# Kernel optimization log

Hardware: AMD Instinct MI355X
Metric: run time of the kernel (lower is better)

## Reference

```python
import jax, jax.numpy as jnp
import numpy as np

# Config mirroring the TF module: cross-attention path (one_on_rna == 2),
# use_attn_augument=1, aug_multiply=0, two_d_softm=1, two_d_softm_mul_row_count=1,
# reduce_level=20 (protok used for padding masks).
B, L, D, H = 4, 1024, 512, 8
DEPTH = D // H          # 64, matches the repeat(64) in padding_to_zeros
NEG = -1.0e9


def setup_inputs() -> dict:
    key = jax.random.key(0)
    ks = jax.random.split(key, 16)
    s = np.float32(1.0 / np.sqrt(D))  # glorot-ish scale
    q = jax.random.normal(ks[0], (B, L, D), jnp.float32)
    kv = jax.random.normal(ks[1], (B, L, D), jnp.float32)
    # protein tokens; 0 == padding (compared against 0.0 in the TF code)
    protok = jax.random.randint(ks[2], (B, L), 0, 21).astype(jnp.float32)
    statpot_hb = jax.random.uniform(ks[3], (B, L, L), dtype=jnp.float32)
    statpot_pi = jax.random.uniform(ks[4], (B, L, L), dtype=jnp.float32)
    # cross padding mask: 1.0 where the protein (query) position is padding
    pad = (protok == 0.0).astype(jnp.float32)            # [B, L]
    cross_mask = jnp.broadcast_to(pad[:, :, None], (B, L, L)).astype(jnp.float32)
    wq = jax.random.normal(ks[5], (D, D), jnp.float32) * s
    wk = jax.random.normal(ks[6], (D, D), jnp.float32) * s
    wv = jax.random.normal(ks[7], (D, D), jnp.float32) * s
    wo = jax.random.normal(ks[8], (D, D), jnp.float32) * s
    bq = jnp.zeros((D,), jnp.float32)
    bk = jnp.zeros((D,), jnp.float32)
    bv = jnp.zeros((D,), jnp.float32)
    bo = jnp.zeros((D,), jnp.float32)
    aug_weight_att = jnp.ones((1,), jnp.float32)
    aug_weight_aug = jnp.ones((1,), jnp.float32)
    return dict(q=q, kv=kv, protok=protok, statpot_hb=statpot_hb,
                statpot_pi=statpot_pi, cross_mask=cross_mask,
                wq=wq, bq=bq, wk=wk, bk=bk, wv=wv, bv=bv, wo=wo, bo=bo,
                aug_weight_att=aug_weight_att, aug_weight_aug=aug_weight_aug)


def _split_heads(x):
    # [B, L, D] -> [B, H, L, depth]
    return x.reshape(B, L, H, DEPTH).transpose(0, 2, 1, 3)


def reference(q, kv, protok, statpot_hb, statpot_pi, cross_mask,
              wq, bq, wk, bk, wv, bv, wo, bo, aug_weight_att, aug_weight_aug):
    # padding_to_zeros: zero features at padded protein positions
    pad_keep = (protok != 0.0).astype(q.dtype)[:, :, None]   # [B, L, 1]
    qp = (q @ wq + bq) * pad_keep   # query side is the protein (len == max_pro_len)
    k = kv @ wk + bk
    v = kv @ wv + bv
    qh, kh, vh = _split_heads(qp), _split_heads(k), _split_heads(v)

    # unscaled QK^T (original does NOT divide by sqrt(depth))
    logits = jnp.einsum('bhqd,bhkd->bhqk', qh, kh)           # [B,H,L,L]

    # statistical-potential augmentation (aug_multiply == 0 -> additive)
    table = jnp.stack([statpot_hb, statpot_pi], axis=1)      # [B,2,L,L]
    table = jnp.repeat(table, H // 2, axis=1)                # [B,H,L,L]
    logits = logits / jnp.max(logits)
    logits = aug_weight_att * logits
    table = aug_weight_aug * table
    table = table / jnp.max(table)
    logits = logits + table

    # additive large-negative mask, broadcast over heads
    logits = logits + cross_mask[:, None, :, :] * NEG

    # 2D softmax jointly over (query, key) axes
    attn = jax.nn.softmax(logits.reshape(B, H, L * L), axis=-1).reshape(B, H, L, L)

    # rescale by number of non-padded protein rows (two_d_softm_mul_row_count)
    mul = jnp.count_nonzero(protok, axis=1).astype(attn.dtype)[:, None, None, None]
    attn = attn * mul
    attn = attn / jnp.max(attn)

    # output = attn^T @ v : contracts the QUERY axis (as in the original matmul)
    out = jnp.einsum('bhqk,bhqd->bhkd', attn, vh)            # [B,H,L,depth]
    out = out.transpose(0, 2, 1, 3).reshape(B, L, D)
    out = out @ wo + bo
    out = out * pad_keep                                     # final padding zeroing
    return out
```

## Files before the change

### kernel.cpp

```cpp
#include <hip/hip_runtime.h>
#include <math.h>

#define BB 4
#define LL 1024
#define DD 512
#define HH 8
#define DEP 64
#define NEGV (-1.0e9f)

typedef __attribute__((ext_vector_type(8))) short bf16x8;
typedef __attribute__((ext_vector_type(4))) float f32x4;
typedef unsigned short u16;
typedef unsigned int u32;

#define S_GMAX 0
#define S_TMAX 1
#define S_TMIN 2
#define S_MUL  4
#define S_SUM  8
#define S_M    40
#define S_C    72
#define P_TMAX 128
#define P_TMIN 384
#define P_GMAX 640
#define SCAL_F 1152
#define PER_T  (BB*HH*LL*DEP)

__device__ inline u16 f2b(float x) {
  u32 u = __float_as_uint(x);
  return (u16)((u + 0x7FFFu + ((u >> 16) & 1u)) >> 16);
}
__device__ inline float b2f(u16 h) { return __uint_as_float(((u32)h) << 16); }

__device__ inline void atomicMaxF(float* addr, float val) {
  unsigned int* ua = (unsigned int*)addr;
  unsigned int old = *ua;
  while (__uint_as_float(old) < val) {
    unsigned int assumed = old;
    old = atomicCAS(ua, assumed, __float_as_uint(val));
    if (old == assumed) break;
  }
}

__global__ void k0_init(float* ws) {
  int t = threadIdx.x;
  if (t < 4)  ws[S_MUL + t] = 0.0f;
  if (t < 32) { ws[S_SUM + t] = 0.0f; ws[S_M + t] = -INFINITY; ws[S_C + t] = 0.0f; }
}

__global__ void k_count(const float* __restrict__ protok, float* ws) {
  int b = blockIdx.x;
  int cnt = 0;
  for (int l = threadIdx.x; l < LL; l += blockDim.x)
    cnt += (protok[b*LL + l] != 0.0f) ? 1 : 0;
  __shared__ int sh[4];
  int lane = threadIdx.x & 63, w = threadIdx.x >> 6;
  #pragma unroll
  for (int o = 32; o > 0; o >>= 1) cnt += __shfl_down(cnt, o);
  if (lane == 0) sh[w] = cnt;
  __syncthreads();
  if (threadIdx.x == 0) ws[S_MUL + b] = (float)(sh[0] + sh[1] + sh[2] + sh[3]);
}

__global__ __launch_bounds__(256) void k_tminmax(const float* __restrict__ hb,
                                                 const float* __restrict__ pi,
                                                 float* __restrict__ ws) {
  const int g = blockIdx.x*256 + threadIdx.x;
  float mx = -INFINITY, mn = INFINITY;
  #pragma unroll
  for (int rep = 0; rep < 4; ++rep) {
    float4 a[4], c[4];
    #pragma unroll
    for (int j = 0; j < 4; ++j) {
      size_t idx = (size_t)rep*262144 + (size_t)j*65536 + g;
      a[j] = ((const float4*)hb)[idx];
      c[j] = ((const float4*)pi)[idx];
    }
    #pragma unroll
    for (int j = 0; j < 4; ++j) {
      mx = fmaxf(mx, fmaxf(fmaxf(a[j].x, a[j].y), fmaxf(a[j].z, a[j].w)));
      mx = fmaxf(mx, fmaxf(fmaxf(c[j].x, c[j].y), fmaxf(c[j].z, c[j].w)));
      mn = fminf(mn, fminf(fminf(a[j].x, a[j].y), fminf(a[j].z, a[j].w)));
      mn = fminf(mn, fminf(fminf(c[j].x, c[j].y), fminf(c[j].z, c[j].w)));
    }
  }
  __shared__ float shx[4], shn[4];
  int lane = threadIdx.x & 63, w = threadIdx.x >> 6;
  #pragma unroll
  for (int o = 32; o > 0; o >>= 1) {
    mx = fmaxf(mx, __shfl_down(mx, o));
    mn = fminf(mn, __shfl_down(mn, o));
  }
  if (lane == 0) { shx[w] = mx; shn[w] = mn; }
  __syncthreads();
  if (threadIdx.x == 0) {
    ws[P_TMAX + blockIdx.x] = fmaxf(fmaxf(shx[0], shx[1]), fmaxf(shx[2], shx[3]));
    ws[P_TMIN + blockIdx.x] = fminf(fminf(shn[0], shn[1]), fminf(shn[2], shn[3]));
  }
}

__global__ void k_red(float* __restrict__ ws) {
  const int t = threadIdx.x;
  float gm = fmaxf(ws[P_GMAX + t], ws[P_GMAX + t + 256]);
  float tm = ws[P_TMAX + t];
  float tn = ws[P_TMIN + t];
  __shared__ float sg[4], st[4], sn[4];
  int lane = t & 63, w = t >> 6;
  #pragma unroll
  for (int o = 32; o > 0; o >>= 1) {
    gm = fmaxf(gm, __shfl_down(gm, o));
    tm = fmaxf(tm, __shfl_down(tm, o));
    tn = fminf(tn, __shfl_down(tn, o));
  }
  if (lane == 0) { sg[w] = gm; st[w] = tm; sn[w] = tn; }
  __syncthreads();
  if (t == 0) {
    ws[S_GMAX] = fmaxf(fmaxf(sg[0], sg[1]), fmaxf(sg[2], sg[3]));
    ws[S_TMAX] = fmaxf(fmaxf(st[0], st[1]), fmaxf(st[2], st[3]));
    ws[S_TMIN] = fminf(fminf(sn[0], sn[1]), fminf(sn[2], sn[3]));
  }
}

__global__ __launch_bounds__(256) void k_xb(const float* __restrict__ q,
                                            const float* __restrict__ kv,
                                            u16* __restrict__ Xb) {
  int tg = blockIdx.x*256 + threadIdx.x;
  int which = tg >> 18;
  size_t off8 = (size_t)(tg & 262143) * 8;
  const float* s = which ? kv : q;
  float4 f0 = *(const float4*)&s[off8];
  float4 f1 = *(const float4*)&s[off8 + 4];
  u32 p0 = (u32)f2b(f0.x) | ((u32)f2b(f0.y) << 16);
  u32 p1 = (u32)f2b(f0.z) | ((u32)f2b(f0.w) << 16);
  u32 p2 = (u32)f2b(f1.x) | ((u32)f2b(f1.y) << 16);
  u32 p3 = (u32)f2b(f1.z) | ((u32)f2b(f1.w) << 16);
  *(int4*)&Xb[(size_t)which*PER_T + off8] = make_int4(p0, p1, p2, p3);
}

__global__ __launch_bounds__(256) void k_wt(
    const float* __restrict__ wq, const float* __restrict__ wk,
    const float* __restrict__ wv, const float* __restrict__ wo,
    u16* __restrict__ WTb) {
  const int g = blockIdx.z;
  const float* W = (g==0)?wq:(g==1)?wk:(g==2)?wv:wo;
  const int k0 = blockIdx.x*64, n0 = blockIdx.y*64;
  __shared__ u16 Ls[64][72];
  const int t = threadIdx.x;
  {
    const int r = t>>2, c16 = (t&3)*16;
    float v[16];
    #pragma unroll
    for (int j=0;j<4;++j) {
      float4 f = *(const float4*)&W[(size_t)(k0+r)*DD + n0 + c16 + 4*j];
      v[4*j]=f.x; v[4*j+1]=f.y; v[4*j+2]=f.z; v[4*j+3]=f.w;
    }
    u32 pk_[8];
    #pragma unroll
    for (int j=0;j<8;++j) pk_[j] = (u32)f2b(v[2*j]) | ((u32)f2b(v[2*j+1])<<16);
    *(int4*)&Ls[r][c16]   = make_int4(pk_[0],pk_[1],pk_[2],pk_[3]);
    *(int4*)&Ls[r][c16+8] = make_int4(pk_[4],pk_[5],pk_[6],pk_[7]);
  }
  __syncthreads();
  {
    const int n = t>>2, kk = (t&3)*16;
    u16 u[16];
    #pragma unroll
    for (int j=0;j<16;++j) u[j] = Ls[kk+j][n];
    u32 q_[8];
    #pragma unroll
    for (int j=0;j<8;++j) q_[j] = (u32)u[2*j] | ((u32)u[2*j+1]<<16);
    size_t dst = ((size_t)(g*DD + n0 + n))*DD + k0 + kk;
    *(int4*)&WTb[dst]   = make_int4(q_[0],q_[1],q_[2],q_[3]);
    *(int4*)&WTb[dst+8] = make_int4(q_[4],q_[5],q_[6],q_[7]);
  }
}

__global__ __launch_bounds__(256) void k1_proj(
    const float* __restrict__ protok,
    const float* __restrict__ bq, const float* __restrict__ bk,
    const float* __restrict__ bv,
    const u16* __restrict__ Xb, const u16* __restrict__ WTb,
    u16* __restrict__ QPb, u16* __restrict__ KHb, u16* __restrict__ VTb) {
  const int gid = blockIdx.z;
  const u16* X = Xb + (gid == 0 ? 0 : (size_t)PER_T);
  const float* bia = (gid == 0) ? bq : (gid == 1) ? bk : bv;
  const int m0 = blockIdx.x*64;
  const int h  = blockIdx.y;
  __shared__ u16 As[64][72];
  __shared__ u16 Bs[64][72];
  const int t = threadIdx.x;
  const int w = t>>6, lane = t&63, i = lane&15, g2 = lane>>4;
  const int sr = t>>2, sc = (t&3)*16;

  f32x4 acc[4];
  #pragma unroll
  for (int ct=0;ct<4;++ct) acc[ct] = (f32x4){0.f,0.f,0.f,0.f};

  for (int kk0 = 0; kk0 < DD; kk0 += 64) {
    __syncthreads();
    {
      size_t sx = (size_t)(m0+sr)*DD + kk0 + sc;
      *(int4*)&As[sr][sc]   = *(const int4*)&X[sx];
      *(int4*)&As[sr][sc+8] = *(const int4*)&X[sx+8];
    }
    {
      size_t src = ((size_t)(gid*DD + h*64 + sr))*DD + kk0 + sc;
      *(int4*)&Bs[sr][sc]   = *(const int4*)&WTb[src];
      *(int4*)&Bs[sr][sc+8] = *(const int4*)&WTb[src+8];
    }
    __syncthreads();
    bf16x8 a0 = *(const bf16x8*)&As[16*w + i][g2*8];
    bf16x8 a1 = *(const bf16x8*)&As[16*w + i][32 + g2*8];
    #pragma unroll
    for (int ct=0; ct<4; ++ct) {
      bf16x8 b0 = *(const bf16x8*)&Bs[ct*16 + i][g2*8];
      bf16x8 b1 = *(const bf16x8*)&Bs[ct*16 + i][32 + g2*8];
      acc[ct] = __builtin_amdgcn_mfma_f32_16x16x32_bf16(a0, b0, acc[ct], 0,0,0);
      acc[ct] = __builtin_amdgcn_mfma_f32_16x16x32_bf16(a1, b1, acc[ct], 0,0,0);
    }
  }
  __syncthreads();
  const int lrow = 16*w + g2*4;
  if (gid == 2) {
    #pragma unroll
    for (int ct=0;ct<4;++ct)
      #pragma unroll
      for (int r=0;r<4;++r)
        As[lrow + r][ct*16 + i] = f2b(acc[ct][r] + bia[h*64 + ct*16 + i]);
    __syncthreads();
    const int b = m0 >> 10, l0 = m0 & 1023;
    const int d = t>>2, lc = (t&3)*16;
    u16 u[16];
    #pragma unroll
    for (int j=0;j<16;++j) u[j] = As[lc+j][d];
    u32 q_[8];
    #pragma unroll
    for (int j=0;j<8;++j) q_[j] = (u32)u[2*j] | ((u32)u[2*j+1]<<16);
    size_t dst = ((size_t)(b*HH + h)*DEP + d)*LL + l0 + lc;
    *(int4*)&VTb[dst]   = make_int4(q_[0],q_[1],q_[2],q_[3]);
    *(int4*)&VTb[dst+8] = make_int4(q_[4],q_[5],q_[6],q_[7]);
  } else {
    u16* Y = (gid == 0) ? QPb : KHb;
    #pragma unroll
    for (int ct=0;ct<4;++ct)
      #pragma unroll
      for (int r=0;r<4;++r) {
        int m = m0 + lrow + r;
        float keep = (gid == 0) ? ((protok[m] != 0.0f) ? 1.0f : 0.0f) : 1.0f;
        int b = m >> 10, l = m & 1023;
        float val = (acc[ct][r] + bia[h*64 + ct*16 + i]) * keep;
        Y[((size_t)(b*HH + h)*LL + l)*DEP + ct*16 + i] = f2b(val);
      }
  }
}

__global__ __launch_bounds__(256) void k3_gmax(
    const u16* __restrict__ QPb, const u16* __restrict__ KHb,
    float* __restrict__ wsf) {
  const int q0 = blockIdx.x*64, bh = blockIdx.y;
  __shared__ u16 Qs[64][72];
  __shared__ u16 Ks[2][64][72];
  const int t = threadIdx.x;
  const int w = t>>6, lane = t&63, i = lane&15, g2 = lane>>4;
  const int sr = t>>2, sc = (t&3)*16;
  const u16* Qb = QPb + (size_t)bh*LL*DEP;
  const u16* Kb = KHb + (size_t)bh*LL*DEP;
  {
    size_t sq = (size_t)(q0 + sr)*DEP + sc;
    *(int4*)&Qs[sr][sc]   = *(const int4*)&Qb[sq];
    *(int4*)&Qs[sr][sc+8] = *(const int4*)&Qb[sq+8];
  }
  int4 rn0 = *(const int4*)&Kb[(size_t)sr*DEP + sc];
  int4 rn1 = *(const int4*)&Kb[(size_t)sr*DEP + sc + 8];
  __syncthreads();
  *(int4*)&Ks[0][sr][sc]   = rn0;
  *(int4*)&Ks[0][sr][sc+8] = rn1;
  rn0 = *(const int4*)&Kb[(size_t)(64 + sr)*DEP + sc];
  rn1 = *(const int4*)&Kb[(size_t)(64 + sr)*DEP + sc + 8];
  __syncthreads();
  bf16x8 a0 = *(const bf16x8*)&Qs[16*w + i][g2*8];
  bf16x8 a1 = *(const bf16x8*)&Qs[16*w + i][32 + g2*8];
  float mx = -INFINITY;
  for (int kt = 0; kt < 16; ++kt) {
    const int cur = kt & 1;
    #pragma unroll
    for (int ct=0;ct<4;++ct) {
      bf16x8 b0 = *(const bf16x8*)&Ks[cur][ct*16 + i][g2*8];
      bf16x8 b1 = *(const bf16x8*)&Ks[cur][ct*16 + i][32 + g2*8];
      f32x4 z = (f32x4){0.f,0.f,0.f,0.f};
      z = __builtin_amdgcn_mfma_f32_16x16x32_bf16(a0, b0, z, 0,0,0);
      z = __builtin_amdgcn_mfma_f32_16x16x32_bf16(a1, b1, z, 0,0,0);
      mx = fmaxf(mx, fmaxf(fmaxf(z[0],z[1]), fmaxf(z[2],z[3])));
    }
    if (kt < 15) {
      __syncthreads();
      *(int4*)&Ks[cur^1][sr][sc]   = rn0;
      *(int4*)&Ks[cur^1][sr][sc+8] = rn1;
      if (kt < 14) {
        rn0 = *(const int4*)&Kb[(size_t)((kt+2)*64 + sr)*DEP + sc];
        rn1 = *(const int4*)&Kb[(size_t)((kt+2)*64 + sr)*DEP + sc + 8];
      }
      __syncthreads();
    }
  }
  __shared__ float red[4];
  #pragma unroll
  for (int o = 32; o > 0; o >>= 1) mx = fmaxf(mx, __shfl_down(mx, o));
  if (lane == 0) red[w] = mx;
  __syncthreads();
  if (t == 0)
    wsf[P_GMAX + bh*16 + blockIdx.x] = fmaxf(fmaxf(red[0],red[1]), fmaxf(red[2],red[3]));
}

__global__ __launch_bounds__(256) void k4_fused(
    const float* __restrict__ protok,
    const float* __restrict__ hb, const float* __restrict__ pi,
    const float* __restrict__ w_att, const float* __restrict__ w_aug,
    const u16* __restrict__ QPb, const u16* __restrict__ KHb,
    const u16* __restrict__ VTb, u16* __restrict__ Ob,
    float* __restrict__ wsf) {
  const int k0 = blockIdx.x*64;
  const int bh = blockIdx.y, b = bh>>3, h = bh&7;
  const float* tab = ((h < 4) ? hb : pi) + (size_t)b*LL*LL;
  const float gmax  = wsf[S_GMAX];
  const float tmaxr = wsf[S_TMAX], tminr = wsf[S_TMIN];
  const float wa = w_att[0], wg = w_aug[0];
  const float inv_g = wa / gmax;
  const float tden  = (wg >= 0.0f) ? (wg * tmaxr) : (wg * tminr);
  const float inv_t = wg / tden;

  __shared__ u16 Ks[64][72];
  __shared__ u16 Qs[64][72];
  __shared__ u16 Vt[64][72];
  __shared__ u16 Pt[64][72];
  const int t = threadIdx.x;
  const int w = t>>6, lane = t&63, i = lane&15, g2 = lane>>4;
  const int sr = t>>2, sc = (t&3)*16;
  const int qlb = 16*w + g2*4;

  {
    size_t sk = ((size_t)bh*LL + k0 + sr)*DEP + sc;
    *(int4*)&Ks[sr][sc]   = *(const int4*)&KHb[sk];
    *(int4*)&Ks[sr][sc+8] = *(const int4*)&KHb[sk+8];
  }
  int4 rq0 = *(const int4*)&QPb[((size_t)bh*LL + sr)*DEP + sc];
  int4 rq1 = *(const int4*)&QPb[((size_t)bh*LL + sr)*DEP + sc + 8];
  int4 rv0 = *(const int4*)&VTb[((size_t)bh*DEP + sr)*LL + sc];
  int4 rv1 = *(const int4*)&VTb[((size_t)bh*DEP + sr)*LL + sc + 8];
  float tvr[4][4];
  #pragma unroll
  for (int r=0;r<4;++r)
    #pragma unroll
    for (int ct=0;ct<4;++ct)
      tvr[r][ct] = tab[(size_t)(qlb + r)*LL + k0 + ct*16 + i];
  __syncthreads();
  bf16x8 kb0[4], kb1[4];
  #pragma unroll
  for (int ct=0;ct<4;++ct) {
    kb0[ct] = *(const bf16x8*)&Ks[ct*16 + i][g2*8];
    kb1[ct] = *(const bf16x8*)&Ks[ct*16 + i][32 + g2*8];
  }
  f32x4 accO[4];
  #pragma unroll
  for (int dt=0;dt<4;++dt) accO[dt] = (f32x4){0.f,0.f,0.f,0.f};
  float lsum = 0.0f, lmax = -INFINITY;

  for (int q0 = 0; q0 < LL; q0 += 64) {
    const bool more = (q0 + 64) < LL;
    __syncthreads();
    *(int4*)&Qs[sr][sc]   = rq0;
    *(int4*)&Qs[sr][sc+8] = rq1;
    *(int4*)&Vt[sr][sc]   = rv0;
    *(int4*)&Vt[sr][sc+8] = rv1;
    __syncthreads();
    if (more) {
      rq0 = *(const int4*)&QPb[((size_t)bh*LL + q0 + 64 + sr)*DEP + sc];
      rq1 = *(const int4*)&QPb[((size_t)bh*LL + q0 + 64 + sr)*DEP + sc + 8];
      rv0 = *(const int4*)&VTb[((size_t)bh*DEP + sr)*LL + q0 + 64 + sc];
      rv1 = *(const int4*)&VTb[((size_t)bh*DEP + sr)*LL + q0 + 64 + sc + 8];
    }
    bf16x8 a0 = *(const bf16x8*)&Qs[16*w + i][g2*8];
    bf16x8 a1 = *(const bf16x8*)&Qs[16*w + i][32 + g2*8];
    f32x4 s4[4];
    #pragma unroll
    for (int ct=0; ct<4; ++ct) {
      f32x4 z = (f32x4){0.f,0.f,0.f,0.f};
      z = __builtin_amdgcn_mfma_f32_16x16x32_bf16(a0, kb0[ct], z, 0,0,0);
      z = __builtin_amdgcn_mfma_f32_16x16x32_bf16(a1, kb1[ct], z, 0,0,0);
      s4[ct] = z;
    }
    float tv2[4][4];
    if (more) {
      #pragma unroll
      for (int r=0;r<4;++r)
        #pragma unroll
        for (int ct=0;ct<4;++ct)
          tv2[r][ct] = tab[(size_t)(q0 + 64 + qlb + r)*LL + k0 + ct*16 + i];
    }
    #pragma unroll
    for (int r=0;r<4;++r) {
      int qrow = q0 + qlb + r;
      float madd = (protok[b*LL + qrow] == 0.0f) ? NEGV : 0.0f;
      #pragma unroll
      for (int ct=0;ct<4;++ct) {
        float sp = s4[ct][r]*inv_g + tvr[r][ct]*inv_t + madd;
        lmax = fmaxf(lmax, sp);
        float p = __expf(sp);
        lsum += p;
        Pt[ct*16 + i][qlb + r] = f2b(p);
      }
    }
    __syncthreads();
    bf16x8 pa0 = *(const bf16x8*)&Pt[16*w + i][g2*8];
    bf16x8 pa1 = *(const bf16x8*)&Pt[16*w + i][32 + g2*8];
    #pragma unroll
    for (int dt=0; dt<4; ++dt) {
      bf16x8 v0 = *(const bf16x8*)&Vt[dt*16 + i][g2*8];
      bf16x8 v1 = *(const bf16x8*)&Vt[dt*16 + i][32 + g2*8];
      accO[dt] = __builtin_amdgcn_mfma_f32_16x16x32_bf16(pa0, v0, accO[dt], 0,0,0);
      accO[dt] = __builtin_amdgcn_mfma_f32_16x16x32_bf16(pa1, v1, accO[dt], 0,0,0);
    }
    if (more) {
      #pragma unroll
      for (int r=0;r<4;++r)
        #pragma unroll
        for (int ct=0;ct<4;++ct) tvr[r][ct] = tv2[r][ct];
    }
  }
  #pragma unroll
  for (int dt=0;dt<4;++dt)
    #pragma unroll
    for (int r=0;r<4;++r)
      Ob[((size_t)bh*LL + k0 + qlb + r)*DEP + dt*16 + i] = f2b(accO[dt][r]);
  __shared__ float rs[4], rm[4];
  #pragma unroll
  for (int o = 32; o > 0; o >>= 1) {
    lsum += __shfl_down(lsum, o);
    lmax = fmaxf(lmax, __shfl_down(lmax, o));
  }
  if (lane == 0) { rs[w] = lsum; rm[w] = lmax; }
  __syncthreads();
  if (t == 0) {
    atomicAdd(&wsf[S_SUM + bh], rs[0]+rs[1]+rs[2]+rs[3]);
    atomicMaxF(&wsf[S_M + bh], fmaxf(fmaxf(rm[0], rm[1]), fmaxf(rm[2], rm[3])));
  }
}

__global__ void k45_cbh(float* ws) {
  int t = threadIdx.x;
  __shared__ float a_sh[32];
  if (t < 32) {
    int b = t >> 3;
    float s = ws[S_SUM + t], m = ws[S_M + t], mul = ws[S_MUL + b];
    a_sh[t] = mul * __expf(m) / s;
  }
  __syncthreads();
  if (t < 32) {
    float amax = -INFINITY;
    #pragma unroll
    for (int i = 0; i < 32; ++i) amax = fmaxf(amax, a_sh[i]);
    int b = t >> 3;
    float s = ws[S_SUM + t], mul = ws[S_MUL + b];
    ws[S_C + t] = (mul / s) / amax;
  }
}

__global__ __launch_bounds__(256) void k5_out(
    const float* __restrict__ protok,
    const float* __restrict__ bo,
    const u16* __restrict__ WTb, const u16* __restrict__ Ob,
    const float* __restrict__ wsf, float* __restrict__ out) {
  const int m0 = blockIdx.x*64, n0 = blockIdx.y*64;
  const int b = m0 >> 10, l0 = m0 & 1023;
  __shared__ u16 As[64][72];
  __shared__ u16 Bs[64][72];
  const int t = threadIdx.x;
  const int w = t>>6, lane = t&63, i = lane&15, g2 = lane>>4;
  const int sr = t>>2, sc = (t&3)*16;
  f32x4 acc[4];
  #pragma unroll
  for (int ct=0;ct<4;++ct) acc[ct] = (f32x4){0.f,0.f,0.f,0.f};

  for (int kk0 = 0; kk0 < DD; kk0 += 64) {
    const int h = kk0 >> 6;
    const float cs = wsf[S_C + b*HH + h];
    __syncthreads();
    {
      union { int4 v[2]; u16 u[16]; } uu;
      size_t so = ((size_t)(b*HH + h)*LL + l0 + sr)*DEP + sc;
      uu.v[0] = *(const int4*)&Ob[so];
      uu.v[1] = *(const int4*)&Ob[so+8];
      u32 pk_[8];
      #pragma unroll
      for (int j=0;j<8;++j)
        pk_[j] = (u32)f2b(b2f(uu.u[2*j])*cs) | ((u32)f2b(b2f(uu.u[2*j+1])*cs)<<16);
      *(int4*)&As[sr][sc]   = make_int4(pk_[0],pk_[1],pk_[2],pk_[3]);
      *(int4*)&As[sr][sc+8] = make_int4(pk_[4],pk_[5],pk_[6],pk_[7]);
    }
    {
      size_t src = ((size_t)(3*DD + n0 + sr))*DD + kk0 + sc;
      *(int4*)&Bs[sr][sc]   = *(const int4*)&WTb[src];
      *(int4*)&Bs[sr][sc+8] = *(const int4*)&WTb[src+8];
    }
    __syncthreads();
    bf16x8 a0 = *(const bf16x8*)&As[16*w + i][g2*8];
    bf16x8 a1 = *(const bf16x8*)&As[16*w + i][32 + g2*8];
    #pragma unroll
    for (int ct=0; ct<4; ++ct) {
      bf16x8 b0 = *(const bf16x8*)&Bs[ct*16 + i][g2*8];
      bf16x8 b1 = *(const bf16x8*)&Bs[ct*16 + i][32 + g2*8];
      acc[ct] = __builtin_amdgcn_mfma_f32_16x16x32_bf16(a0, b0, acc[ct], 0,0,0);
      acc[ct] = __builtin_amdgcn_mfma_f32_16x16x32_bf16(a1, b1, acc[ct], 0,0,0);
    }
  }
  #pragma unroll
  for (int ct=0;ct<4;++ct)
    #pragma unroll
    for (int r=0;r<4;++r) {
      int m = m0 + 16*w + g2*4 + r;
      float keep = (protok[m] != 0.0f) ? 1.0f : 0.0f;
      out[(size_t)m*DD + n0 + ct*16 + i] = (acc[ct][r] + bo[n0 + ct*16 + i]) * keep;
    }
}

extern "C" void kernel_launch(void* const* d_in, const int* in_sizes, int n_in,
                              void* d_out, int out_size, void* d_ws, size_t ws_size,
                              hipStream_t stream) {
  const float* q      = (const float*)d_in[0];
  const float* kv     = (const float*)d_in[1];
  const float* protok = (const float*)d_in[2];
  const float* hb     = (const float*)d_in[3];
  const float* pi     = (const float*)d_in[4];
  const float* wq = (const float*)d_in[6];
  const float* bq = (const float*)d_in[7];
  const float* wk = (const float*)d_in[8];
  const float* bk = (const float*)d_in[9];
  const float* wv = (const float*)d_in[10];
  const float* bv = (const float*)d_in[11];
  const float* wo = (const float*)d_in[12];
  const float* bo = (const float*)d_in[13];
  const float* w_att = (const float*)d_in[14];
  const float* w_aug = (const float*)d_in[15];
  float* wsf = (float*)d_ws;
  float* out = (float*)d_out;

  u16* base = (u16*)(wsf + SCAL_F);
  u16* QPb = base;
  u16* KHb = QPb + PER_T;
  u16* VTb = KHb + PER_T;
  u16* Ob  = VTb + PER_T;
  u16* WTb = Ob  + PER_T;
  u16* Xb  = WTb + 4*DD*DD;

  k0_init   <<<1, 64, 0, stream>>>(wsf);
  k_count   <<<4, 256, 0, stream>>>(protok, wsf);
  k_tminmax <<<256, 256, 0, stream>>>(hb, pi, wsf);
  k_xb      <<<2048, 256, 0, stream>>>(q, kv, Xb);
  k_wt      <<<dim3(8, 8, 4), 256, 0, stream>>>(wq, wk, wv, wo, WTb);
  k1_proj   <<<dim3(64, 8, 3), 256, 0, stream>>>(protok, bq, bk, bv, Xb, WTb, QPb, KHb, VTb);
  k3_gmax   <<<dim3(16, 32), 256, 0, stream>>>(QPb, KHb, wsf);
  k_red     <<<1, 256, 0, stream>>>(wsf);
  k4_fused  <<<dim3(16, 32), 256, 0, stream>>>(protok, hb, pi, w_att, w_aug,
                                               QPb, KHb, VTb, Ob, wsf);
  k45_cbh   <<<1, 64, 0, stream>>>(wsf);
  k5_out    <<<dim3(64, 8), 256, 0, stream>>>(protok, bo, WTb, Ob, wsf, out);
}
```

Baseline: 211.5 us.

## Split attention over query halves and merge small kernels to cut launches

```diff
diff --git a/kernel.cpp b/kernel.cpp
--- a/kernel.cpp
+++ b/kernel.cpp
@@ -13,17 +13,15 @@
 typedef unsigned short u16;
 typedef unsigned int u32;
 
-#define S_GMAX 0
 #define S_TMAX 1
 #define S_TMIN 2
 #define S_MUL  4
 #define S_SUM  8
 #define S_M    40
-#define S_C    72
 #define P_TMAX 128
 #define P_TMIN 384
 #define P_GMAX 640
-#define SCAL_F 1152
+#define SCAL_F 1792
 #define PER_T  (BB*HH*LL*DEP)
 
 __device__ inline u16 f2b(float x) {
@@ -42,30 +40,28 @@
   }
 }
 
-__global__ void k0_init(float* ws) {
-  int t = threadIdx.x;
-  if (t < 4)  ws[S_MUL + t] = 0.0f;
-  if (t < 32) { ws[S_SUM + t] = 0.0f; ws[S_M + t] = -INFINITY; ws[S_C + t] = 0.0f; }
-}
-
-__global__ void k_count(const float* __restrict__ protok, float* ws) {
-  int b = blockIdx.x;
-  int cnt = 0;
-  for (int l = threadIdx.x; l < LL; l += blockDim.x)
-    cnt += (protok[b*LL + l] != 0.0f) ? 1 : 0;
-  __shared__ int sh[4];
-  int lane = threadIdx.x & 63, w = threadIdx.x >> 6;
-  #pragma unroll
-  for (int o = 32; o > 0; o >>= 1) cnt += __shfl_down(cnt, o);
-  if (lane == 0) sh[w] = cnt;
-  __syncthreads();
-  if (threadIdx.x == 0) ws[S_MUL + b] = (float)(sh[0] + sh[1] + sh[2] + sh[3]);
-}
-
 __global__ __launch_bounds__(256) void k_tminmax(const float* __restrict__ hb,
                                                  const float* __restrict__ pi,
+                                                 const float* __restrict__ protok,
                                                  float* __restrict__ ws) {
-  const int g = blockIdx.x*256 + threadIdx.x;
+  const int t = threadIdx.x;
+  if (blockIdx.x == 4 && t < 32) {
+    ws[S_SUM + t] = 0.0f; ws[S_M + t] = -INFINITY;
+  }
+  if (blockIdx.x < 4) {
+    int b = blockIdx.x;
+    int cnt = 0;
+    for (int l = t; l < LL; l += 256)
+      cnt += (protok[b*LL + l] != 0.0f) ? 1 : 0;
+    __shared__ int shc[4];
+    int lane = t & 63, w = t >> 6;
+    #pragma unroll
+    for (int o = 32; o > 0; o >>= 1) cnt += __shfl_down(cnt, o);
+    if (lane == 0) shc[w] = cnt;
+    __syncthreads();
+    if (t == 0) ws[S_MUL + b] = (float)(shc[0] + shc[1] + shc[2] + shc[3]);
+  }
+  const int g = blockIdx.x*256 + t;
   float mx = -INFINITY, mn = INFINITY;
   #pragma unroll
   for (int rep = 0; rep < 4; ++rep) {
@@ -85,7 +81,7 @@
     }
   }
   __shared__ float shx[4], shn[4];
-  int lane = threadIdx.x & 63, w = threadIdx.x >> 6;
+  int lane = t & 63, w = t >> 6;
   #pragma unroll
   for (int o = 32; o > 0; o >>= 1) {
     mx = fmaxf(mx, __shfl_down(mx, o));
@@ -93,85 +89,80 @@
   }
   if (lane == 0) { shx[w] = mx; shn[w] = mn; }
   __syncthreads();
-  if (threadIdx.x == 0) {
+  if (t == 0) {
     ws[P_TMAX + blockIdx.x] = fmaxf(fmaxf(shx[0], shx[1]), fmaxf(shx[2], shx[3]));
     ws[P_TMIN + blockIdx.x] = fminf(fminf(shn[0], shn[1]), fminf(shn[2], shn[3]));
   }
 }
 
-__global__ void k_red(float* __restrict__ ws) {
-  const int t = threadIdx.x;
-  float gm = fmaxf(ws[P_GMAX + t], ws[P_GMAX + t + 256]);
-  float tm = ws[P_TMAX + t];
-  float tn = ws[P_TMIN + t];
-  __shared__ float sg[4], st[4], sn[4];
-  int lane = t & 63, w = t >> 6;
-  #pragma unroll
-  for (int o = 32; o > 0; o >>= 1) {
-    gm = fmaxf(gm, __shfl_down(gm, o));
-    tm = fmaxf(tm, __shfl_down(tm, o));
-    tn = fminf(tn, __shfl_down(tn, o));
-  }
-  if (lane == 0) { sg[w] = gm; st[w] = tm; sn[w] = tn; }
-  __syncthreads();
-  if (t == 0) {
-    ws[S_GMAX] = fmaxf(fmaxf(sg[0], sg[1]), fmaxf(sg[2], sg[3]));
-    ws[S_TMAX] = fmaxf(fmaxf(st[0], st[1]), fmaxf(st[2], st[3]));
-    ws[S_TMIN] = fminf(fminf(sn[0], sn[1]), fminf(sn[2], sn[3]));
-  }
-}
-
-__global__ __launch_bounds__(256) void k_xb(const float* __restrict__ q,
-                                            const float* __restrict__ kv,
-                                            u16* __restrict__ Xb) {
-  int tg = blockIdx.x*256 + threadIdx.x;
-  int which = tg >> 18;
-  size_t off8 = (size_t)(tg & 262143) * 8;
-  const float* s = which ? kv : q;
-  float4 f0 = *(const float4*)&s[off8];
-  float4 f1 = *(const float4*)&s[off8 + 4];
-  u32 p0 = (u32)f2b(f0.x) | ((u32)f2b(f0.y) << 16);
-  u32 p1 = (u32)f2b(f0.z) | ((u32)f2b(f0.w) << 16);
-  u32 p2 = (u32)f2b(f1.x) | ((u32)f2b(f1.y) << 16);
-  u32 p3 = (u32)f2b(f1.z) | ((u32)f2b(f1.w) << 16);
-  *(int4*)&Xb[(size_t)which*PER_T + off8] = make_int4(p0, p1, p2, p3);
-}
-
-__global__ __launch_bounds__(256) void k_wt(
+__global__ __launch_bounds__(256) void k_prep(
+    const float* __restrict__ q, const float* __restrict__ kv,
     const float* __restrict__ wq, const float* __restrict__ wk,
     const float* __restrict__ wv, const float* __restrict__ wo,
-    u16* __restrict__ WTb) {
-  const int g = blockIdx.z;
-  const float* W = (g==0)?wq:(g==1)?wk:(g==2)?wv:wo;
-  const int k0 = blockIdx.x*64, n0 = blockIdx.y*64;
-  __shared__ u16 Ls[64][72];
+    u16* __restrict__ Xb, u16* __restrict__ WTb, float* __restrict__ ws) {
+  const int bid = blockIdx.x;
   const int t = threadIdx.x;
-  {
-    const int r = t>>2, c16 = (t&3)*16;
-    float v[16];
-    #pragma unroll
-    for (int j=0;j<4;++j) {
-      float4 f = *(const float4*)&W[(size_t)(k0+r)*DD + n0 + c16 + 4*j];
-      v[4*j]=f.x; v[4*j+1]=f.y; v[4*j+2]=f.z; v[4*j+3]=f.w;
-    }
-    u32 pk_[8];
-    #pragma unroll
-    for (int j=0;j<8;++j) pk_[j] = (u32)f2b(v[2*j]) | ((u32)f2b(v[2*j+1])<<16);
-    *(int4*)&Ls[r][c16]   = make_int4(pk_[0],pk_[1],pk_[2],pk_[3]);
-    *(int4*)&Ls[r][c16+8] = make_int4(pk_[4],pk_[5],pk_[6],pk_[7]);
-  }
-  __syncthreads();
-  {
-    const int n = t>>2, kk = (t&3)*16;
-    u16 u[16];
-    #pragma unroll
-    for (int j=0;j<16;++j) u[j] = Ls[kk+j][n];
-    u32 q_[8];
-    #pragma unroll
-    for (int j=0;j<8;++j) q_[j] = (u32)u[2*j] | ((u32)u[2*j+1]<<16);
-    size_t dst = ((size_t)(g*DD + n0 + n))*DD + k0 + kk;
-    *(int4*)&WTb[dst]   = make_int4(q_[0],q_[1],q_[2],q_[3]);
-    *(int4*)&WTb[dst+8] = make_int4(q_[4],q_[5],q_[6],q_[7]);
+  if (bid < 2048) {
+    int tg = bid*256 + t;
+    int which = tg >> 18;
+    size_t off8 = (size_t)(tg & 262143) * 8;
+    const float* s = which ? kv : q;
+    float4 f0 = *(const float4*)&s[off8];
+    float4 f1 = *(const float4*)&s[off8 + 4];
+    u32 p0 = (u32)f2b(f0.x) | ((u32)f2b(f0.y) << 16);
+    u32 p1 = (u32)f2b(f0.z) | ((u32)f2b(f0.w) << 16);
+    u32 p2 = (u32)f2b(f1.x) | ((u32)f2b(f1.y) << 16);
+    u32 p3 = (u32)f2b(f1.z) | ((u32)f2b(f1.w) << 16);
+    *(int4*)&Xb[(size_t)which*PER_T + off8] = make_int4(p0, p1, p2, p3);
+  } else if (bid < 2304) {
+    const int wid = bid - 2048;
+    const int g = wid >> 6, rem = wid & 63;
+    const int k0 = (rem >> 3)*64, n0 = (rem & 7)*64;
+    const float* W = (g==0)?wq:(g==1)?wk:(g==2)?wv:wo;
+    __shared__ u16 Ls[64][72];
+    {
+      const int r = t>>2, c16 = (t&3)*16;
+      float v[16];
+      #pragma unroll
+      for (int j=0;j<4;++j) {
+        float4 f = *(const float4*)&W[(size_t)(k0+r)*DD + n0 + c16 + 4*j];
+        v[4*j]=f.x; v[4*j+1]=f.y; v[4*j+2]=f.z; v[4*j+3]=f.w;
+      }
+      u32 pk_[8];
+      #pragma unroll
+      for (int j=0;j<8;++j) pk_[j] = (u32)f2b(v[2*j]) | ((u32)f2b(v[2*j+1])<<16);
+      *(int4*)&Ls[r][c16]   = make_int4(pk_[0],pk_[1],pk_[2],pk_[3]);
+      *(int4*)&Ls[r][c16+8] = make_int4(pk_[4],pk_[5],pk_[6],pk_[7]);
+    }
+    __syncthreads();
+    {
+      const int n = t>>2, kk = (t&3)*16;
+      u16 u[16];
+      #pragma unroll
+      for (int j=0;j<16;++j) u[j] = Ls[kk+j][n];
+      u32 q_[8];
+      #pragma unroll
+      for (int j=0;j<8;++j) q_[j] = (u32)u[2*j] | ((u32)u[2*j+1]<<16);
+      size_t dst = ((size_t)(g*DD + n0 + n))*DD + k0 + kk;
+      *(int4*)&WTb[dst]   = make_int4(q_[0],q_[1],q_[2],q_[3]);
+      *(int4*)&WTb[dst+8] = make_int4(q_[4],q_[5],q_[6],q_[7]);
+    }
+  } else {
+    float tm = ws[P_TMAX + t];
+    float tn = ws[P_TMIN + t];
+    __shared__ float st[4], sn[4];
+    int lane = t & 63, w = t >> 6;
+    #pragma unroll
+    for (int o = 32; o > 0; o >>= 1) {
+      tm = fmaxf(tm, __shfl_down(tm, o));
+      tn = fminf(tn, __shfl_down(tn, o));
+    }
+    if (lane == 0) { st[w] = tm; sn[w] = tn; }
+    __syncthreads();
+    if (t == 0) {
+      ws[S_TMAX] = fmaxf(fmaxf(st[0], st[1]), fmaxf(st[2], st[3]));
+      ws[S_TMIN] = fminf(fminf(sn[0], sn[1]), fminf(sn[2], sn[3]));
+    }
   }
 }
 
@@ -257,48 +248,57 @@
 __global__ __launch_bounds__(256) void k3_gmax(
     const u16* __restrict__ QPb, const u16* __restrict__ KHb,
     float* __restrict__ wsf) {
-  const int q0 = blockIdx.x*64, bh = blockIdx.y;
-  __shared__ u16 Qs[64][72];
+  const int q0 = blockIdx.x*128, bh = blockIdx.y, kz = blockIdx.z;
+  __shared__ u16 Qs[2][64][72];
   __shared__ u16 Ks[2][64][72];
   const int t = threadIdx.x;
   const int w = t>>6, lane = t&63, i = lane&15, g2 = lane>>4;
   const int sr = t>>2, sc = (t&3)*16;
   const u16* Qb = QPb + (size_t)bh*LL*DEP;
   const u16* Kb = KHb + (size_t)bh*LL*DEP;
-  {
-    size_t sq = (size_t)(q0 + sr)*DEP + sc;
-    *(int4*)&Qs[sr][sc]   = *(const int4*)&Qb[sq];
-    *(int4*)&Qs[sr][sc+8] = *(const int4*)&Qb[sq+8];
-  }
-  int4 rn0 = *(const int4*)&Kb[(size_t)sr*DEP + sc];
-  int4 rn1 = *(const int4*)&Kb[(size_t)sr*DEP + sc + 8];
+  #pragma unroll
+  for (int qs = 0; qs < 2; ++qs) {
+    size_t sq = (size_t)(q0 + qs*64 + sr)*DEP + sc;
+    *(int4*)&Qs[qs][sr][sc]   = *(const int4*)&Qb[sq];
+    *(int4*)&Qs[qs][sr][sc+8] = *(const int4*)&Qb[sq+8];
+  }
+  const int kb = kz*4;
+  int4 rn0 = *(const int4*)&Kb[(size_t)(kb*64 + sr)*DEP + sc];
+  int4 rn1 = *(const int4*)&Kb[(size_t)(kb*64 + sr)*DEP + sc + 8];
   __syncthreads();
   *(int4*)&Ks[0][sr][sc]   = rn0;
   *(int4*)&Ks[0][sr][sc+8] = rn1;
-  rn0 = *(const int4*)&Kb[(size_t)(64 + sr)*DEP + sc];
-  rn1 = *(const int4*)&Kb[(size_t)(64 + sr)*DEP + sc + 8];
-  __syncthreads();
-  bf16x8 a0 = *(const bf16x8*)&Qs[16*w + i][g2*8];
-  bf16x8 a1 = *(const bf16x8*)&Qs[16*w + i][32 + g2*8];
+  rn0 = *(const int4*)&Kb[(size_t)((kb+1)*64 + sr)*DEP + sc];
+  rn1 = *(const int4*)&Kb[(size_t)((kb+1)*64 + sr)*DEP + sc + 8];
+  __syncthreads();
+  bf16x8 a0[2], a1[2];
+  #pragma unroll
+  for (int qs = 0; qs < 2; ++qs) {
+    a0[qs] = *(const bf16x8*)&Qs[qs][16*w + i][g2*8];
+    a1[qs] = *(const bf16x8*)&Qs[qs][16*w + i][32 + g2*8];
+  }
   float mx = -INFINITY;
-  for (int kt = 0; kt < 16; ++kt) {
+  for (int kt = 0; kt < 4; ++kt) {
     const int cur = kt & 1;
     #pragma unroll
     for (int ct=0;ct<4;++ct) {
       bf16x8 b0 = *(const bf16x8*)&Ks[cur][ct*16 + i][g2*8];
       bf16x8 b1 = *(const bf16x8*)&Ks[cur][ct*16 + i][32 + g2*8];
-      f32x4 z = (f32x4){0.f,0.f,0.f,0.f};
-      z = __builtin_amdgcn_mfma_f32_16x16x32_bf16(a0, b0, z, 0,0,0);
-      z = __builtin_amdgcn_mfma_f32_16x16x32_bf16(a1, b1, z, 0,0,0);
-      mx = fmaxf(mx, fmaxf(fmaxf(z[0],z[1]), fmaxf(z[2],z[3])));
-    }
-    if (kt < 15) {
+      #pragma unroll
+      for (int qs=0;qs<2;++qs) {
+        f32x4 z = (f32x4){0.f,0.f,0.f,0.f};
+        z = __builtin_amdgcn_mfma_f32_16x16x32_bf16(a0[qs], b0, z, 0,0,0);
+        z = __builtin_amdgcn_mfma_f32_16x16x32_bf16(a1[qs], b1, z, 0,0,0);
+        mx = fmaxf(mx, fmaxf(fmaxf(z[0],z[1]), fmaxf(z[2],z[3])));
+      }
+    }
+    if (kt < 3) {
       __syncthreads();
       *(int4*)&Ks[cur^1][sr][sc]   = rn0;
       *(int4*)&Ks[cur^1][sr][sc+8] = rn1;
-      if (kt < 14) {
-        rn0 = *(const int4*)&Kb[(size_t)((kt+2)*64 + sr)*DEP + sc];
-        rn1 = *(const int4*)&Kb[(size_t)((kt+2)*64 + sr)*DEP + sc + 8];
+      if (kt < 2) {
+        rn0 = *(const int4*)&Kb[(size_t)((kb+kt+2)*64 + sr)*DEP + sc];
+        rn1 = *(const int4*)&Kb[(size_t)((kb+kt+2)*64 + sr)*DEP + sc + 8];
       }
       __syncthreads();
     }
@@ -309,7 +309,8 @@
   if (lane == 0) red[w] = mx;
   __syncthreads();
   if (t == 0)
-    wsf[P_GMAX + bh*16 + blockIdx.x] = fmaxf(fmaxf(red[0],red[1]), fmaxf(red[2],red[3]));
+    wsf[P_GMAX + (bh*8 + blockIdx.x)*4 + kz] =
+        fmaxf(fmaxf(red[0],red[1]), fmaxf(red[2],red[3]));
 }
 
 __global__ __launch_bounds__(256) void k4_fused(
@@ -317,43 +318,57 @@
     const float* __restrict__ hb, const float* __restrict__ pi,
     const float* __restrict__ w_att, const float* __restrict__ w_aug,
     const u16* __restrict__ QPb, const u16* __restrict__ KHb,
-    const u16* __restrict__ VTb, u16* __restrict__ Ob,
+    const u16* __restrict__ VTb,
+    u16* __restrict__ Ob0, u16* __restrict__ Ob1,
     float* __restrict__ wsf) {
   const int k0 = blockIdx.x*64;
   const int bh = blockIdx.y, b = bh>>3, h = bh&7;
+  const int qbase = blockIdx.z * 512;
+  u16* Obz = blockIdx.z ? Ob1 : Ob0;
   const float* tab = ((h < 4) ? hb : pi) + (size_t)b*LL*LL;
-  const float gmax  = wsf[S_GMAX];
+  const int t = threadIdx.x;
+  const int w = t>>6, lane = t&63, i = lane&15, g2 = lane>>4;
+  const int sr = t>>2, sc = (t&3)*16;
+  const int qlb = 16*w + g2*4;
+
+  __shared__ float gsh;
+  {
+    float gm = -INFINITY;
+    #pragma unroll
+    for (int j=0;j<4;++j) gm = fmaxf(gm, wsf[P_GMAX + j*256 + t]);
+    __shared__ float red[4];
+    #pragma unroll
+    for (int o = 32; o > 0; o >>= 1) gm = fmaxf(gm, __shfl_down(gm, o));
+    if (lane == 0) red[w] = gm;
+    __syncthreads();
+    if (t == 0) gsh = fmaxf(fmaxf(red[0],red[1]), fmaxf(red[2],red[3]));
+  }
   const float tmaxr = wsf[S_TMAX], tminr = wsf[S_TMIN];
   const float wa = w_att[0], wg = w_aug[0];
-  const float inv_g = wa / gmax;
-  const float tden  = (wg >= 0.0f) ? (wg * tmaxr) : (wg * tminr);
+  const float tden = (wg >= 0.0f) ? (wg * tmaxr) : (wg * tminr);
   const float inv_t = wg / tden;
 
   __shared__ u16 Ks[64][72];
   __shared__ u16 Qs[64][72];
   __shared__ u16 Vt[64][72];
   __shared__ u16 Pt[64][72];
-  const int t = threadIdx.x;
-  const int w = t>>6, lane = t&63, i = lane&15, g2 = lane>>4;
-  const int sr = t>>2, sc = (t&3)*16;
-  const int qlb = 16*w + g2*4;
-
   {
     size_t sk = ((size_t)bh*LL + k0 + sr)*DEP + sc;
     *(int4*)&Ks[sr][sc]   = *(const int4*)&KHb[sk];
     *(int4*)&Ks[sr][sc+8] = *(const int4*)&KHb[sk+8];
   }
-  int4 rq0 = *(const int4*)&QPb[((size_t)bh*LL + sr)*DEP + sc];
-  int4 rq1 = *(const int4*)&QPb[((size_t)bh*LL + sr)*DEP + sc + 8];
-  int4 rv0 = *(const int4*)&VTb[((size_t)bh*DEP + sr)*LL + sc];
-  int4 rv1 = *(const int4*)&VTb[((size_t)bh*DEP + sr)*LL + sc + 8];
+  int4 rq0 = *(const int4*)&QPb[((size_t)bh*LL + qbase + sr)*DEP + sc];
+  int4 rq1 = *(const int4*)&QPb[((size_t)bh*LL + qbase + sr)*DEP + sc + 8];
+  int4 rv0 = *(const int4*)&VTb[((size_t)bh*DEP + sr)*LL + qbase + sc];
+  int4 rv1 = *(const int4*)&VTb[((size_t)bh*DEP + sr)*LL + qbase + sc + 8];
   float tvr[4][4];
   #pragma unroll
   for (int r=0;r<4;++r)
     #pragma unroll
     for (int ct=0;ct<4;++ct)
-      tvr[r][ct] = tab[(size_t)(qlb + r)*LL + k0 + ct*16 + i];
-  __syncthreads();
+      tvr[r][ct] = tab[(size_t)(qbase + qlb + r)*LL + k0 + ct*16 + i];
+  __syncthreads();
+  const float inv_g = wa / gsh;
   bf16x8 kb0[4], kb1[4];
   #pragma unroll
   for (int ct=0;ct<4;++ct) {
@@ -365,8 +380,8 @@
   for (int dt=0;dt<4;++dt) accO[dt] = (f32x4){0.f,0.f,0.f,0.f};
   float lsum = 0.0f, lmax = -INFINITY;
 
-  for (int q0 = 0; q0 < LL; q0 += 64) {
-    const bool more = (q0 + 64) < LL;
+  for (int q0 = qbase; q0 < qbase + 512; q0 += 64) {
+    const bool more = (q0 + 64) < (qbase + 512);
     __syncthreads();
     *(int4*)&Qs[sr][sc]   = rq0;
     *(int4*)&Qs[sr][sc+8] = rq1;
@@ -397,18 +412,24 @@
         for (int ct=0;ct<4;++ct)
           tv2[r][ct] = tab[(size_t)(q0 + 64 + qlb + r)*LL + k0 + ct*16 + i];
     }
-    #pragma unroll
-    for (int r=0;r<4;++r) {
-      int qrow = q0 + qlb + r;
-      float madd = (protok[b*LL + qrow] == 0.0f) ? NEGV : 0.0f;
-      #pragma unroll
-      for (int ct=0;ct<4;++ct) {
-        float sp = s4[ct][r]*inv_g + tvr[r][ct]*inv_t + madd;
+    float madd[4];
+    #pragma unroll
+    for (int r=0;r<4;++r)
+      madd[r] = (protok[b*LL + q0 + qlb + r] == 0.0f) ? NEGV : 0.0f;
+    #pragma unroll
+    for (int ct=0;ct<4;++ct) {
+      float pr[4];
+      #pragma unroll
+      for (int r=0;r<4;++r) {
+        float sp = fmaf(s4[ct][r], inv_g, fmaf(tvr[r][ct], inv_t, madd[r]));
         lmax = fmaxf(lmax, sp);
         float p = __expf(sp);
         lsum += p;
-        Pt[ct*16 + i][qlb + r] = f2b(p);
+        pr[r] = p;
       }
+      u32 pk0 = (u32)f2b(pr[0]) | ((u32)f2b(pr[1])<<16);
+      u32 pk1 = (u32)f2b(pr[2]) | ((u32)f2b(pr[3])<<16);
+      *(uint2*)&Pt[ct*16 + i][qlb] = make_uint2(pk0, pk1);
     }
     __syncthreads();
     bf16x8 pa0 = *(const bf16x8*)&Pt[16*w + i][g2*8];
@@ -431,7 +452,7 @@
   for (int dt=0;dt<4;++dt)
     #pragma unroll
     for (int r=0;r<4;++r)
-      Ob[((size_t)bh*LL + k0 + qlb + r)*DEP + dt*16 + i] = f2b(accO[dt][r]);
+      Obz[((size_t)bh*LL + k0 + qlb + r)*DEP + dt*16 + i] = f2b(accO[dt][r]);
   __shared__ float rs[4], rm[4];
   #pragma unroll
   for (int o = 32; o > 0; o >>= 1) {
@@ -446,54 +467,54 @@
   }
 }
 
-__global__ void k45_cbh(float* ws) {
-  int t = threadIdx.x;
-  __shared__ float a_sh[32];
-  if (t < 32) {
-    int b = t >> 3;
-    float s = ws[S_SUM + t], m = ws[S_M + t], mul = ws[S_MUL + b];
-    a_sh[t] = mul * __expf(m) / s;
-  }
-  __syncthreads();
-  if (t < 32) {
-    float amax = -INFINITY;
-    #pragma unroll
-    for (int i = 0; i < 32; ++i) amax = fmaxf(amax, a_sh[i]);
-    int b = t >> 3;
-    float s = ws[S_SUM + t], mul = ws[S_MUL + b];
-    ws[S_C + t] = (mul / s) / amax;
-  }
-}
-
 __global__ __launch_bounds__(256) void k5_out(
     const float* __restrict__ protok,
     const float* __restrict__ bo,
-    const u16* __restrict__ WTb, const u16* __restrict__ Ob,
+    const u16* __restrict__ WTb,
+    const u16* __restrict__ O0, const u16* __restrict__ O1,
     const float* __restrict__ wsf, float* __restrict__ out) {
   const int m0 = blockIdx.x*64, n0 = blockIdx.y*64;
   const int b = m0 >> 10, l0 = m0 & 1023;
   __shared__ u16 As[64][72];
   __shared__ u16 Bs[64][72];
+  __shared__ float csh[8];
   const int t = threadIdx.x;
   const int w = t>>6, lane = t&63, i = lane&15, g2 = lane>>4;
   const int sr = t>>2, sc = (t&3)*16;
+
+  __shared__ float ash[32];
+  if (t < 32)
+    ash[t] = wsf[S_MUL + (t>>3)] * __expf(wsf[S_M + t]) / wsf[S_SUM + t];
+  __syncthreads();
+  if (t < 8) {
+    float amax = -INFINITY;
+    #pragma unroll
+    for (int j = 0; j < 32; ++j) amax = fmaxf(amax, ash[j]);
+    csh[t] = (wsf[S_MUL + b] / wsf[S_SUM + b*HH + t]) / amax;
+  }
+
   f32x4 acc[4];
   #pragma unroll
   for (int ct=0;ct<4;++ct) acc[ct] = (f32x4){0.f,0.f,0.f,0.f};
 
   for (int kk0 = 0; kk0 < DD; kk0 += 64) {
     const int h = kk0 >> 6;
-    const float cs = wsf[S_C + b*HH + h];
     __syncthreads();
     {
-      union { int4 v[2]; u16 u[16]; } uu;
+      union { int4 v[2]; u16 u[16]; } u0, u1;
       size_t so = ((size_t)(b*HH + h)*LL + l0 + sr)*DEP + sc;
-      uu.v[0] = *(const int4*)&Ob[so];
-      uu.v[1] = *(const int4*)&Ob[so+8];
+      u0.v[0] = *(const int4*)&O0[so];
+      u0.v[1] = *(const int4*)&O0[so+8];
+      u1.v[0] = *(const int4*)&O1[so];
+      u1.v[1] = *(const int4*)&O1[so+8];
+      const float cs = csh[h];
       u32 pk_[8];
       #pragma unroll
-      for (int j=0;j<8;++j)
-        pk_[j] = (u32)f2b(b2f(uu.u[2*j])*cs) | ((u32)f2b(b2f(uu.u[2*j+1])*cs)<<16);
+      for (int j=0;j<8;++j) {
+        float lo = (b2f(u0.u[2*j])   + b2f(u1.u[2*j]))   * cs;
+        float hi = (b2f(u0.u[2*j+1]) + b2f(u1.u[2*j+1])) * cs;
+        pk_[j] = (u32)f2b(lo) | ((u32)f2b(hi)<<16);
+      }
       *(int4*)&As[sr][sc]   = make_int4(pk_[0],pk_[1],pk_[2],pk_[3]);
       *(int4*)&As[sr][sc+8] = make_int4(pk_[4],pk_[5],pk_[6],pk_[7]);
     }
@@ -548,20 +569,17 @@
   u16* QPb = base;
   u16* KHb = QPb + PER_T;
   u16* VTb = KHb + PER_T;
-  u16* Ob  = VTb + PER_T;
-  u16* WTb = Ob  + PER_T;
-  u16* Xb  = WTb + 4*DD*DD;
-
-  k0_init   <<<1, 64, 0, stream>>>(wsf);
-  k_count   <<<4, 256, 0, stream>>>(protok, wsf);
-  k_tminmax <<<256, 256, 0, stream>>>(hb, pi, wsf);
-  k_xb      <<<2048, 256, 0, stream>>>(q, kv, Xb);
-  k_wt      <<<dim3(8, 8, 4), 256, 0, stream>>>(wq, wk, wv, wo, WTb);
+  u16* XO  = VTb + PER_T;
+  u16* WTb = XO  + 2*PER_T;
+  u16* Xb  = XO;
+  u16* Ob0 = XO;
+  u16* Ob1 = XO + PER_T;
+
+  k_tminmax <<<256, 256, 0, stream>>>(hb, pi, protok, wsf);
+  k_prep    <<<2305, 256, 0, stream>>>(q, kv, wq, wk, wv, wo, Xb, WTb, wsf);
   k1_proj   <<<dim3(64, 8, 3), 256, 0, stream>>>(protok, bq, bk, bv, Xb, WTb, QPb, KHb, VTb);
-  k3_gmax   <<<dim3(16, 32), 256, 0, stream>>>(QPb, KHb, wsf);
-  k_red     <<<1, 256, 0, stream>>>(wsf);
-  k4_fused  <<<dim3(16, 32), 256, 0, stream>>>(protok, hb, pi, w_att, w_aug,
-                                               QPb, KHb, VTb, Ob, wsf);
-  k45_cbh   <<<1, 64, 0, stream>>>(wsf);
-  k5_out    <<<dim3(64, 8), 256, 0, stream>>>(protok, bo, WTb, Ob, wsf, out);
-}
+  k3_gmax   <<<dim3(8, 32, 4), 256, 0, stream>>>(QPb, KHb, wsf);
+  k4_fused  <<<dim3(16, 32, 2), 256, 0, stream>>>(protok, hb, pi, w_att, w_aug,
+                                                  QPb, KHb, VTb, Ob0, Ob1, wsf);
+  k5_out    <<<dim3(64, 8), 256, 0, stream>>>(protok, bo, WTb, Ob0, Ob1, wsf, out);
+}
```

Measured after the change: 215.3 us. No clear change (+1.8%).
